# Kernel optimization log

Hardware: AMD Instinct MI355X
Metric: run time of the kernel (lower is better)

The kernel has to match this reference:

```python
import jax, jax.numpy as jnp
import numpy as np

HEADS = 8
DIM_HEAD = 64


def layernorm(x, g, b, eps=1e-5):
    mu = x.mean(axis=-1, keepdims=True)
    var = ((x - mu) ** 2).mean(axis=-1, keepdims=True)
    return (x - mu) * jax.lax.rsqrt(var + eps) * g + b


def setup_inputs() -> dict:
    key = jax.random.key(0)
    ks = jax.random.split(key, 8)
    B, N, D = 1, 896, 3072          # batch, enformer bins, enformer_hidden_dim
    C, J, CD = 64, 1, 2560          # num context tracks, kv len per track, context_dim
    INNER = HEADS * DIM_HEAD        # 512
    return {
        'embeddings': jax.random.normal(ks[0], (B, N, D), jnp.float32),
        'context': jax.random.normal(ks[1], (C, J, CD), jnp.float32),
        'context_mask': jnp.ones((C, J), dtype=bool),
        'qn_g': jnp.ones((D,), jnp.float32),
        'qn_b': jnp.zeros((D,), jnp.float32),
        'kn_g': jnp.ones((CD,), jnp.float32),
        'kn_b': jnp.zeros((CD,), jnp.float32),
        'Wq': jax.random.normal(ks[2], (D, INNER), jnp.float32) / np.sqrt(D),
        'Wkv': jax.random.normal(ks[3], (CD, 2 * INNER), jnp.float32) / np.sqrt(CD),
        'null_k': jax.random.normal(ks[4], (INNER,), jnp.float32),
        'null_v': jax.random.normal(ks[5], (INNER,), jnp.float32),
        'Wo': jax.random.normal(ks[6], (INNER, D), jnp.float32) / np.sqrt(INNER),
        'bo': jnp.zeros((D,), jnp.float32),
        'Wp': jax.random.normal(ks[7], (D, 1), jnp.float32) / np.sqrt(D),
        'bp': jnp.zeros((1,), jnp.float32),
    }


def reference(embeddings, context, context_mask, qn_g, qn_b, kn_g, kn_b,
              Wq, Wkv, null_k, null_v, Wo, bo, Wp, bp):
    h, dh = HEADS, DIM_HEAD
    scale = dh ** -0.5
    b, n, d = embeddings.shape
    c, j, _ = context.shape

    q = layernorm(embeddings, qn_g, qn_b) @ Wq                  # (b, n, h*dh)
    kv = layernorm(context, kn_g, kn_b) @ Wkv                   # (c, j, 2*h*dh)
    k, v = jnp.split(kv, 2, axis=-1)

    # null key/value concat along kv-sequence dim
    nk = jnp.broadcast_to(null_k, (c, 1, h * dh))
    nv = jnp.broadcast_to(null_v, (c, 1, h * dh))
    k = jnp.concatenate([nk, k], axis=1)                        # (c, j+1, h*dh)
    v = jnp.concatenate([nv, v], axis=1)

    q = q.reshape(b, n, h, dh).transpose(0, 2, 1, 3)            # (b, h, i, dh)
    k = k.reshape(c, j + 1, h, dh).transpose(0, 2, 1, 3)        # (c, h, j+1, dh)
    v = v.reshape(c, j + 1, h, dh).transpose(0, 2, 1, 3)

    sim = jnp.einsum('bhid,chjd->bchij', q, k) * scale          # (b, c, h, i, j+1)
    mask = jnp.pad(context_mask, ((0, 0), (1, 0)), constant_values=True)  # (c, j+1)
    sim = jnp.where(mask[None, :, None, None, :], sim, -jnp.finfo(sim.dtype).max)
    attn = jax.nn.softmax(sim, axis=-1)

    out = jnp.einsum('bchij,chjd->bchid', attn, v)              # (b, c, h, i, dh)
    out = out.transpose(0, 1, 3, 2, 4).reshape(b, c, n, h * dh)

    branch = out @ Wo + bo                                      # (b, c, n, d)
    emb2 = embeddings[:, None] + branch                         # residual (b==1 broadcast)

    pred = (emb2 @ Wp + bp)[..., 0]                             # (b, c, n)
    pred = jax.nn.softplus(pred).transpose(0, 2, 1)             # 'b c n 1 -> b n c'
    return pred
```

## Files before the change

### kernel.cpp

```cpp
#include <hip/hip_runtime.h>
#include <hip/hip_bf16.h>
#include <cstddef>

#define N_  896
#define D_  3072
#define C_  64
#define CD_ 2560
#define INNER_ 512
#define HEADS_ 8
#define ZQ_ 8
#define ZKV_ 8

typedef __attribute__((ext_vector_type(8))) short short8;
typedef __attribute__((ext_vector_type(4))) float f32x4;

__device__ __forceinline__ void split_bf16(float x, unsigned short& hi, unsigned short& lo)
{
    unsigned u = __float_as_uint(x);
    hi = (unsigned short)(u >> 16);
    float xh = __uint_as_float(u & 0xffff0000u);
    lo = (unsigned short)(__float_as_uint(x - xh) >> 16);
}

__global__ __launch_bounds__(256) void stats_wowp(
    const float* __restrict__ emb, const float* __restrict__ ctx,
    const float* __restrict__ Wp,  const float* __restrict__ Wo,
    const float* __restrict__ bo,  const float* __restrict__ bp,
    float2* __restrict__ statsE, float2* __restrict__ statsC,
    float* __restrict__ ep, float* __restrict__ WoWp, float* __restrict__ c0)
{
    const int bid = blockIdx.x;
    const int t = threadIdx.x;
    const int wave = t >> 6, lane = t & 63;
    __shared__ float sm[8];

    if (bid >= N_ + C_) {
        if (bid == N_ + C_ + 128) {
            float s = 0.f;
            for (int f = t; f < D_; f += 256) s += bo[f] * Wp[f];
#pragma unroll
            for (int off = 32; off > 0; off >>= 1) s += __shfl_xor(s, off);
            if (lane == 0) sm[wave] = s;
            __syncthreads();
            if (t == 0) c0[0] = sm[0] + sm[1] + sm[2] + sm[3] + bp[0];
        } else {
            const int row = (bid - (N_ + C_)) * 4 + wave;
            const float4* a4 = (const float4*)(Wo + (size_t)row * D_);
            const float4* w4 = (const float4*)Wp;
            float s = 0.f;
#pragma unroll
            for (int i = 0; i < 12; ++i) {
                const int f = lane + 64 * i;
                float4 a = a4[f], w = w4[f];
                s += a.x * w.x + a.y * w.y + a.z * w.z + a.w * w.w;
            }
#pragma unroll
            for (int off = 32; off > 0; off >>= 1) s += __shfl_xor(s, off);
            if (lane == 0) WoWp[row] = s;
        }
        return;
    }

    const bool isE = bid < N_;
    const int row = isE ? bid : bid - N_;
    const int ncols = isE ? D_ : CD_;
    const float* X = isE ? emb + (size_t)row * D_ : ctx + (size_t)row * CD_;
    const int nf4 = ncols >> 2;
    const float4* x4 = (const float4*)X;
    float4 xs[3];
    float sum = 0.f, dotp = 0.f;
#pragma unroll
    for (int i = 0; i < 3; ++i) {
        const int f = t + 256 * i;
        if (f < nf4) {
            float4 v = x4[f];
            xs[i] = v;
            sum += (v.x + v.y) + (v.z + v.w);
            if (isE) {
                float4 w = ((const float4*)Wp)[f];
                dotp += v.x * w.x + v.y * w.y + v.z * w.z + v.w * w.w;
            }
        }
    }
#pragma unroll
    for (int off = 32; off > 0; off >>= 1) {
        sum  += __shfl_xor(sum, off);
        dotp += __shfl_xor(dotp, off);
    }
    if (lane == 0) { sm[wave] = sum; sm[4 + wave] = dotp; }
    __syncthreads();
    sum  = sm[0] + sm[1] + sm[2] + sm[3];
    dotp = sm[4] + sm[5] + sm[6] + sm[7];
    const float mu = sum / (float)ncols;

    float sq = 0.f;
#pragma unroll
    for (int i = 0; i < 3; ++i) {
        const int f = t + 256 * i;
        if (f < nf4) {
            float4 v = xs[i];
            float a = v.x - mu, b2 = v.y - mu, c = v.z - mu, d = v.w - mu;
            sq += a * a + b2 * b2 + c * c + d * d;
        }
    }
#pragma unroll
    for (int off = 32; off > 0; off >>= 1) sq += __shfl_xor(sq, off);
    __syncthreads();
    if (lane == 0) sm[wave] = sq;
    __syncthreads();
    sq = sm[0] + sm[1] + sm[2] + sm[3];
    const float rstd = rsqrtf(sq / (float)ncols + 1e-5f);
    if (t == 0) {
        float2 st = make_float2(rstd, -mu * rstd);
        if (isE) { statsE[row] = st; ep[row] = dotp; }
        else     { statsC[row] = st; }
    }
}

__global__ __launch_bounds__(256) void gemms(
    const float* __restrict__ emb, const float2* __restrict__ statsE,
    const float* __restrict__ qg, const float* __restrict__ qb,
    const float* __restrict__ Wq, float* __restrict__ qpart,
    const float* __restrict__ ctx, const float2* __restrict__ statsC,
    const float* __restrict__ kg, const float* __restrict__ kb,
    const float* __restrict__ Wkv, float* __restrict__ kp)
{
    __shared__ __align__(16) char smem[44032];
    const int i = blockIdx.x;
    const int t = threadIdx.x;

    if (i < 224) {
        unsigned short (*Ah)[40] = (unsigned short (*)[40])(smem);
        unsigned short (*Al)[40] = (unsigned short (*)[40])(smem + 10240);
        unsigned short (*Bh)[40] = (unsigned short (*)[40])(smem + 20480);
        unsigned short (*Bl)[40] = (unsigned short (*)[40])(smem + 30720);
        float* gsl = (float*)(smem + 40960);
        float* bsl = gsl + 384;

        const int bz = i & 7, sp = i >> 3;
        const int bx = sp & 3, by = sp >> 2;
        const int m0 = by * 128, n0 = bx * 128, k0 = bz * 384;
        if (t < 96) {
            ((float4*)gsl)[t] = ((const float4*)(qg + k0))[t];
            ((float4*)bsl)[t] = ((const float4*)(qb + k0))[t];
        }
        const int ar = t >> 1;
        const int akk = (t & 1) << 4;
        const float2 st = statsE[m0 + ar];
        const int brp = t & 15;
        const int bn0 = (t >> 4) << 3;
        const int l = t & 63;
        const int w = t >> 6;
        const int wm = (w >> 1) << 6;
        const int wn = (w & 1) << 6;
        const int kk0 = (l >> 4) << 3;
        const int li = l & 15;

        const float* aP = emb + (size_t)(m0 + ar) * D_ + k0 + akk;
        const float* bP = Wq + (size_t)(k0 + 2 * brp) * INNER_ + n0 + bn0;
        float4 aR[4];
        float4 bRa0 = *(const float4*)bP;
        float4 bRa1 = *(const float4*)(bP + 4);
        float4 bRb0 = *(const float4*)(bP + INNER_);
        float4 bRb1 = *(const float4*)(bP + INNER_ + 4);
#pragma unroll
        for (int j = 0; j < 4; ++j) aR[j] = *(const float4*)(aP + 4 * j);

        f32x4 acc[4][4] = {};

        for (int itn = 0; itn < 12; ++itn) {
            __syncthreads();
            const int kbase = itn * 32 + akk;
#pragma unroll
            for (int j = 0; j < 4; ++j) {
                float xe[4] = {aR[j].x, aR[j].y, aR[j].z, aR[j].w};
                unsigned short h[4], lo[4];
#pragma unroll
                for (int e = 0; e < 4; ++e) {
                    const int kidx = kbase + 4 * j + e;
                    float x = (xe[e] * st.x + st.y) * gsl[kidx] + bsl[kidx];
                    split_bf16(x, h[e], lo[e]);
                }
                uint2 ph = make_uint2((unsigned)h[0] | ((unsigned)h[1] << 16),
                                      (unsigned)h[2] | ((unsigned)h[3] << 16));
                uint2 pl = make_uint2((unsigned)lo[0] | ((unsigned)lo[1] << 16),
                                      (unsigned)lo[2] | ((unsigned)lo[3] << 16));
                *(uint2*)&Ah[ar][akk + 4 * j] = ph;
                *(uint2*)&Al[ar][akk + 4 * j] = pl;
            }
            {
                float x0e[8] = {bRa0.x, bRa0.y, bRa0.z, bRa0.w, bRa1.x, bRa1.y, bRa1.z, bRa1.w};
                float x1e[8] = {bRb0.x, bRb0.y, bRb0.z, bRb0.w, bRb1.x, bRb1.y, bRb1.z, bRb1.w};
#pragma unroll
                for (int j = 0; j < 8; ++j) {
                    unsigned short h0, l0, h1, l1;
                    split_bf16(x0e[j], h0, l0);
                    split_bf16(x1e[j], h1, l1);
                    *(unsigned*)&Bh[bn0 + j][2 * brp] = (unsigned)h0 | ((unsigned)h1 << 16);
                    *(unsigned*)&Bl[bn0 + j][2 * brp] = (unsigned)l0 | ((unsigned)l1 << 16);
                }
            }
            if (itn < 11) {
                aP += 32;
                bP += (size_t)32 * INNER_;
                bRa0 = *(const float4*)bP;
                bRa1 = *(const float4*)(bP + 4);
                bRb0 = *(const float4*)(bP + INNER_);
                bRb1 = *(const float4*)(bP + INNER_ + 4);
#pragma unroll
                for (int j = 0; j < 4; ++j) aR[j] = *(const float4*)(aP + 4 * j);
            }
            __syncthreads();
            short8 bhf[4], blf[4];
#pragma unroll
            for (int fn = 0; fn < 4; ++fn) {
                const int rn = wn + fn * 16 + li;
                bhf[fn] = *(const short8*)&Bh[rn][kk0];
                blf[fn] = *(const short8*)&Bl[rn][kk0];
            }
#pragma unroll
            for (int fm = 0; fm < 4; ++fm) {
                const int rm = wm + fm * 16 + li;
                short8 ah = *(const short8*)&Ah[rm][kk0];
                short8 al = *(const short8*)&Al[rm][kk0];
#pragma unroll
                for (int fn = 0; fn < 4; ++fn) {
                    acc[fm][fn] = __builtin_amdgcn_mfma_f32_16x16x32_bf16(ah, bhf[fn], acc[fm][fn], 0, 0, 0);
                    acc[fm][fn] = __builtin_amdgcn_mfma_f32_16x16x32_bf16(ah, blf[fn], acc[fm][fn], 0, 0, 0);
                    acc[fm][fn] = __builtin_amdgcn_mfma_f32_16x16x32_bf16(al, bhf[fn], acc[fm][fn], 0, 0, 0);
                }
            }
        }
        float* Cp = qpart + (size_t)bz * (N_ * INNER_);
#pragma unroll
        for (int fm = 0; fm < 4; ++fm) {
            const int rbase = m0 + wm + fm * 16 + ((l >> 4) << 2);
#pragma unroll
            for (int fn = 0; fn < 4; ++fn) {
                const int col = n0 + wn + fn * 16 + li;
#pragma unroll
                for (int jj = 0; jj < 4; ++jj)
                    Cp[(size_t)(rbase + jj) * INNER_ + col] = acc[fm][fn][jj];
            }
        }
        return;
    }

    float (*As)[68] = (float (*)[68])(smem);
    float (*Bs)[68] = (float (*)[68])(smem + 8704);
    float* gs  = (float*)(smem + 17408);
    float* bs2 = gs + 320;
    const int j2 = i - 224;
    const int bz = j2 & 7;
    const int bx = j2 >> 3;
    const int n0 = bx * 64, k0 = bz * 320;
    float* Cc = kp + (size_t)bz * (C_ * 1024);

    for (int f = t; f < 80; f += 256) {
        ((float4*)gs)[f]  = ((const float4*)(kg + k0))[f];
        ((float4*)bs2)[f] = ((const float4*)(kb + k0))[f];
    }
    const int ar = t >> 2;
    const int ac = (t & 3) * 8;
    const float2 st = statsC[ar];
    const int bk = t >> 3;
    const int bn = (t & 7) * 8;
    const int tm = (t >> 4) * 4, tn = (t & 15) * 4;
    float acc[4][4] = {};

    for (int kt = k0; kt < k0 + 320; kt += 32) {
        const float* ap = ctx + (size_t)ar * CD_ + kt + ac;
        float4 a0 = *(const float4*)ap;
        float4 a1 = *(const float4*)(ap + 4);
        const float* bp2 = Wkv + (size_t)(kt + bk) * 1024 + n0 + bn;
        float4 b0 = *(const float4*)bp2;
        float4 b1 = *(const float4*)(bp2 + 4);
        __syncthreads();
        const int kr2 = kt - k0 + ac;
        float4 g0 = *(const float4*)&gs[kr2];
        float4 g1 = *(const float4*)&gs[kr2 + 4];
        float4 c0v = *(const float4*)&bs2[kr2];
        float4 c1v = *(const float4*)&bs2[kr2 + 4];
        As[ac + 0][ar] = (a0.x * st.x + st.y) * g0.x + c0v.x;
        As[ac + 1][ar] = (a0.y * st.x + st.y) * g0.y + c0v.y;
        As[ac + 2][ar] = (a0.z * st.x + st.y) * g0.z + c0v.z;
        As[ac + 3][ar] = (a0.w * st.x + st.y) * g0.w + c0v.w;
        As[ac + 4][ar] = (a1.x * st.x + st.y) * g1.x + c1v.x;
        As[ac + 5][ar] = (a1.y * st.x + st.y) * g1.y + c1v.y;
        As[ac + 6][ar] = (a1.z * st.x + st.y) * g1.z + c1v.z;
        As[ac + 7][ar] = (a1.w * st.x + st.y) * g1.w + c1v.w;
        *(float4*)&Bs[bk][bn]     = b0;
        *(float4*)&Bs[bk][bn + 4] = b1;
        __syncthreads();
#pragma unroll
        for (int kk = 0; kk < 32; ++kk) {
            float4 av = *(const float4*)&As[kk][tm];
            float4 bv = *(const float4*)&Bs[kk][tn];
            acc[0][0] += av.x * bv.x; acc[0][1] += av.x * bv.y;
            acc[0][2] += av.x * bv.z; acc[0][3] += av.x * bv.w;
            acc[1][0] += av.y * bv.x; acc[1][1] += av.y * bv.y;
            acc[1][2] += av.y * bv.z; acc[1][3] += av.y * bv.w;
            acc[2][0] += av.z * bv.x; acc[2][1] += av.z * bv.y;
            acc[2][2] += av.z * bv.z; acc[2][3] += av.z * bv.w;
            acc[3][0] += av.w * bv.x; acc[3][1] += av.w * bv.y;
            acc[3][2] += av.w * bv.z; acc[3][3] += av.w * bv.w;
        }
    }
#pragma unroll
    for (int r = 0; r < 4; ++r)
        *(float4*)(Cc + (size_t)(tm + r) * 1024 + n0 + tn) =
            make_float4(acc[r][0], acc[r][1], acc[r][2], acc[r][3]);
}

__global__ __launch_bounds__(256) void kred_vp(
    const float* __restrict__ kp, const float* __restrict__ WoWp,
    const float* __restrict__ null_v, float* __restrict__ kvb,
    float* __restrict__ vp, float* __restrict__ nvp)
{
    const int c = blockIdx.x;
    const int t = threadIdx.x;
#pragma unroll
    for (int n = t; n < 512; n += 256) {
        float s = 0.f;
#pragma unroll
        for (int z = 0; z < ZKV_; ++z) s += kp[(size_t)z * (C_ * 1024) + c * 1024 + n];
        kvb[c * 512 + n] = s;
    }
    const int w = t >> 6, lane = t & 63;
#pragma unroll
    for (int half = 0; half < 2; ++half) {
        const int jj = half * 256 + w * 64 + lane;
        float s = 0.f;
#pragma unroll
        for (int z = 0; z < ZKV_; ++z) s += kp[(size_t)z * (C_ * 1024) + c * 1024 + 512 + jj];
        float x = s * WoWp[jj];
#pragma unroll
        for (int off = 32; off > 0; off >>= 1) x += __shfl_xor(x, off);
        if (lane == 0) vp[c * 8 + half * 4 + w] = x;
    }
    if (c == 0) {
#pragma unroll
        for (int half = 0; half < 2; ++half) {
            const int jj = half * 256 + w * 64 + lane;
            float x = null_v[jj] * WoWp[jj];
#pragma unroll
            for (int off = 32; off > 0; off >>= 1) x += __shfl_xor(x, off);
            if (lane == 0) nvp[half * 4 + w] = x;
        }
    }
}

__global__ __launch_bounds__(512) void attn_pred(
    const float* __restrict__ qp, const float* __restrict__ kvb,
    const float* __restrict__ vp, const float* __restrict__ nvp,
    const float* __restrict__ nk, const float* __restrict__ ep,
    const float* __restrict__ c0p, const unsigned char* __restrict__ msk,
    float* __restrict__ out)
{
    const int t = threadIdx.x;
    const int n0 = blockIdx.x * 4;
    const size_t MN = (size_t)N_ * INNER_;
    __shared__ float q_lds[4][8][68];
    __shared__ float s0_lds[4][8];
#pragma unroll
    for (int nn = 0; nn < 4; ++nn) {
        const size_t base = (size_t)(n0 + nn) * INNER_ + t;
        float v = 0.f;
#pragma unroll
        for (int z = 0; z < ZQ_; ++z) v += qp[z * MN + base];
        q_lds[nn][t >> 6][t & 63] = v;
    }
    __syncthreads();
    if (t < 32) {
        const int nn = t >> 3, h = t & 7;
        const float* qq = &q_lds[nn][h][0];
        float s = 0.f;
#pragma unroll
        for (int d = 0; d < 64; ++d) s += qq[d] * nk[h * 64 + d];
        s0_lds[nn][h] = s * 0.125f;
    }
    __syncthreads();
    const int c = t >> 3, h = t & 7;
    const bool mv = (msk[c] != 0) || (msk[4 * c] != 0);
    float kreg[64];
    {
        const float4* k4 = (const float4*)(kvb + c * 512 + h * 64);
#pragma unroll
        for (int i = 0; i < 16; ++i) {
            float4 v = k4[i];
            kreg[4 * i] = v.x; kreg[4 * i + 1] = v.y;
            kreg[4 * i + 2] = v.z; kreg[4 * i + 3] = v.w;
        }
    }
    const float vpch = vp[c * 8 + h];
    const float nvph = nvp[h];
    const float c0 = c0p[0];
#pragma unroll
    for (int nn = 0; nn < 4; ++nn) {
        const float* qq = &q_lds[nn][h][0];
        float s = 0.f;
#pragma unroll
        for (int d = 0; d < 64; ++d) s += qq[d] * kreg[d];
        s *= 0.125f;
        float a1 = mv ? 1.f / (1.f + expf(s0_lds[nn][h] - s)) : 0.f;
        float contrib = nvph + a1 * (vpch - nvph);
        contrib += __shfl_xor(contrib, 1);
        contrib += __shfl_xor(contrib, 2);
        contrib += __shfl_xor(contrib, 4);
        if (h == 0) {
            float x = ep[n0 + nn] + c0 + contrib;
            out[(size_t)(n0 + nn) * 64 + c] = fmaxf(x, 0.f) + log1pf(expf(-fabsf(x)));
        }
    }
}

extern "C" void kernel_launch(void* const* d_in, const int* in_sizes, int n_in,
                              void* d_out, int out_size, void* d_ws, size_t ws_size,
                              hipStream_t stream)
{
    const float* emb    = (const float*)d_in[0];
    const float* ctx    = (const float*)d_in[1];
    const unsigned char* msk = (const unsigned char*)d_in[2];
    const float* qn_g   = (const float*)d_in[3];
    const float* qn_b   = (const float*)d_in[4];
    const float* kn_g   = (const float*)d_in[5];
    const float* kn_b   = (const float*)d_in[6];
    const float* Wq     = (const float*)d_in[7];
    const float* Wkv    = (const float*)d_in[8];
    const float* null_k = (const float*)d_in[9];
    const float* null_v = (const float*)d_in[10];
    const float* Wo     = (const float*)d_in[11];
    const float* bo     = (const float*)d_in[12];
    const float* Wp     = (const float*)d_in[13];
    const float* bp     = (const float*)d_in[14];
    float* out = (float*)d_out;

    float* ws    = (float*)d_ws;
    float* qpart = ws;
    float* kp    = qpart + (size_t)ZQ_ * N_ * INNER_;
    float* kvb   = kp + (size_t)ZKV_ * C_ * 1024;
    float* e_p   = kvb + (size_t)C_ * 512;
    float* WoWp  = e_p + N_;
    float* vp    = WoWp + INNER_;
    float* nvp   = vp + C_ * HEADS_;
    float* c0    = nvp + HEADS_;
    float2* statsE = (float2*)(c0 + 1);
    float2* statsC = statsE + N_;

    stats_wowp<<<N_ + C_ + 128 + 1, 256, 0, stream>>>(
        emb, ctx, Wp, Wo, bo, bp, statsE, statsC, e_p, WoWp, c0);
    gemms<<<224 + 16 * ZKV_, 256, 0, stream>>>(
        emb, statsE, qn_g, qn_b, Wq, qpart,
        ctx, statsC, kn_g, kn_b, Wkv, kp);
    kred_vp<<<C_, 256, 0, stream>>>(kp, WoWp, null_v, kvb, vp, nvp);
    attn_pred<<<N_ / 4, 512, 0, stream>>>(qpart, kvb, vp, nvp, null_k,
                                          e_p, c0, msk, out);
}
```

Baseline: 140.7 us.

## Move context KV projection onto split-bf16 MFMA path with shared GEMM helper

The context LayerNorm+Wkv projection, previously a scalar FP32 SIMT GEMM with 128 blocks at 8-way split-K, now reuses the same 3-pass split-bf16 MFMA routine as the query projection. It runs as 32 blocks of 128x128 tiles with 4-way split-K and rows clamped and masked for the 64 real rows. The bf16 hi/lo split also switches from truncation to round-to-nearest-even. The KV tiles waste half their MFMA work on padding rows, and the grid shrinks to 256 blocks.

Measured after the change: 157.4 us. 11.9% more time.

```diff
diff --git a/kernel.cpp b/kernel.cpp
--- a/kernel.cpp
+++ b/kernel.cpp
@@ -9,17 +9,19 @@
 #define INNER_ 512
 #define HEADS_ 8
 #define ZQ_ 8
-#define ZKV_ 8
+#define ZKV_ 4
 
 typedef __attribute__((ext_vector_type(8))) short short8;
 typedef __attribute__((ext_vector_type(4))) float f32x4;
 
-__device__ __forceinline__ void split_bf16(float x, unsigned short& hi, unsigned short& lo)
+__device__ __forceinline__ void split_bf16_rne(float x, unsigned short& hi, unsigned short& lo)
 {
     unsigned u = __float_as_uint(x);
-    hi = (unsigned short)(u >> 16);
-    float xh = __uint_as_float(u & 0xffff0000u);
-    lo = (unsigned short)(__float_as_uint(x - xh) >> 16);
+    unsigned short h = (unsigned short)((u + 0x7fffu + ((u >> 16) & 1u)) >> 16);
+    float xh = __uint_as_float((unsigned)h << 16);
+    unsigned ur = __float_as_uint(x - xh);
+    unsigned short l2 = (unsigned short)((ur + 0x7fffu + ((ur >> 16) & 1u)) >> 16);
+    hi = h; lo = l2;
 }
 
 __global__ __launch_bounds__(256) void stats_wowp(
@@ -117,6 +119,128 @@
     }
 }
 
+__device__ __forceinline__ void mfma_gemm_ln(
+    char* smem, int t,
+    const float* __restrict__ A, int lda, const float2* __restrict__ stats, int Mreal,
+    const float* __restrict__ gv, const float* __restrict__ bv,
+    const float* __restrict__ Bm, int ldb,
+    float* __restrict__ Cp, int ldc,
+    int m0, int n0, int k0, int iters)
+{
+    unsigned short (*Ah)[40] = (unsigned short (*)[40])(smem);
+    unsigned short (*Al)[40] = (unsigned short (*)[40])(smem + 10240);
+    unsigned short (*Bh)[40] = (unsigned short (*)[40])(smem + 20480);
+    unsigned short (*Bl)[40] = (unsigned short (*)[40])(smem + 30720);
+    float* gsl = (float*)(smem + 40960);
+    float* bsl = gsl + 640;
+
+    for (int f = t; f < iters * 8; f += 256) {
+        ((float4*)gsl)[f] = ((const float4*)(gv + k0))[f];
+        ((float4*)bsl)[f] = ((const float4*)(bv + k0))[f];
+    }
+    const int ar  = t >> 1;
+    const int akk = (t & 1) << 4;
+    const int arow = min(m0 + ar, Mreal - 1);
+    const float2 st = stats[arow];
+    const int brp = t & 15;
+    const int bn0 = (t >> 4) << 3;
+    const int l  = t & 63;
+    const int w  = t >> 6;
+    const int wm = (w >> 1) << 6;
+    const int wn = (w & 1) << 6;
+    const int kk0 = (l >> 4) << 3;
+    const int li  = l & 15;
+
+    const float* aP = A + (size_t)arow * lda + k0 + akk;
+    const float* bP = Bm + (size_t)(k0 + 2 * brp) * ldb + n0 + bn0;
+    float4 aR[4], bR[4];
+    bR[0] = *(const float4*)bP;
+    bR[1] = *(const float4*)(bP + 4);
+    bR[2] = *(const float4*)(bP + ldb);
+    bR[3] = *(const float4*)(bP + ldb + 4);
+#pragma unroll
+    for (int j = 0; j < 4; ++j) aR[j] = *(const float4*)(aP + 4 * j);
+
+    f32x4 acc[4][4] = {};
+
+    for (int itn = 0; itn < iters; ++itn) {
+        __syncthreads();
+        const int kbase = itn * 32 + akk;
+#pragma unroll
+        for (int j = 0; j < 4; ++j) {
+            float xe[4] = {aR[j].x, aR[j].y, aR[j].z, aR[j].w};
+            unsigned short h[4], lo[4];
+#pragma unroll
+            for (int e = 0; e < 4; ++e) {
+                const int kidx = kbase + 4 * j + e;
+                float x = (xe[e] * st.x + st.y) * gsl[kidx] + bsl[kidx];
+                split_bf16_rne(x, h[e], lo[e]);
+            }
+            uint2 ph = make_uint2((unsigned)h[0] | ((unsigned)h[1] << 16),
+                                  (unsigned)h[2] | ((unsigned)h[3] << 16));
+            uint2 pl = make_uint2((unsigned)lo[0] | ((unsigned)lo[1] << 16),
+                                  (unsigned)lo[2] | ((unsigned)lo[3] << 16));
+            *(uint2*)&Ah[ar][akk + 4 * j] = ph;
+            *(uint2*)&Al[ar][akk + 4 * j] = pl;
+        }
+        {
+            float x0e[8] = {bR[0].x, bR[0].y, bR[0].z, bR[0].w, bR[1].x, bR[1].y, bR[1].z, bR[1].w};
+            float x1e[8] = {bR[2].x, bR[2].y, bR[2].z, bR[2].w, bR[3].x, bR[3].y, bR[3].z, bR[3].w};
+#pragma unroll
+            for (int j = 0; j < 8; ++j) {
+                unsigned short h0, l0, h1, l1;
+                split_bf16_rne(x0e[j], h0, l0);
+                split_bf16_rne(x1e[j], h1, l1);
+                *(unsigned*)&Bh[bn0 + j][2 * brp] = (unsigned)h0 | ((unsigned)h1 << 16);
+                *(unsigned*)&Bl[bn0 + j][2 * brp] = (unsigned)l0 | ((unsigned)l1 << 16);
+            }
+        }
+        if (itn < iters - 1) {
+            aP += 32;
+            bP += (size_t)32 * ldb;
+            bR[0] = *(const float4*)bP;
+            bR[1] = *(const float4*)(bP + 4);
+            bR[2] = *(const float4*)(bP + ldb);
+            bR[3] = *(const float4*)(bP + ldb + 4);
+#pragma unroll
+            for (int j = 0; j < 4; ++j) aR[j] = *(const float4*)(aP + 4 * j);
+        }
+        __syncthreads();
+        short8 bhf[4], blf[4];
+#pragma unroll
+        for (int fn = 0; fn < 4; ++fn) {
+            const int rn = wn + fn * 16 + li;
+            bhf[fn] = *(const short8*)&Bh[rn][kk0];
+            blf[fn] = *(const short8*)&Bl[rn][kk0];
+        }
+#pragma unroll
+        for (int fm = 0; fm < 4; ++fm) {
+            const int rm = wm + fm * 16 + li;
+            short8 ah = *(const short8*)&Ah[rm][kk0];
+            short8 al = *(const short8*)&Al[rm][kk0];
+#pragma unroll
+            for (int fn = 0; fn < 4; ++fn) {
+                acc[fm][fn] = __builtin_amdgcn_mfma_f32_16x16x32_bf16(ah, bhf[fn], acc[fm][fn], 0, 0, 0);
+                acc[fm][fn] = __builtin_amdgcn_mfma_f32_16x16x32_bf16(ah, blf[fn], acc[fm][fn], 0, 0, 0);
+                acc[fm][fn] = __builtin_amdgcn_mfma_f32_16x16x32_bf16(al, bhf[fn], acc[fm][fn], 0, 0, 0);
+            }
+        }
+    }
+#pragma unroll
+    for (int fm = 0; fm < 4; ++fm) {
+        const int trow = wm + fm * 16 + ((l >> 4) << 2);
+        if (m0 + trow < Mreal) {
+#pragma unroll
+            for (int fn = 0; fn < 4; ++fn) {
+                const int col = n0 + wn + fn * 16 + li;
+#pragma unroll
+                for (int jj = 0; jj < 4; ++jj)
+                    Cp[(size_t)(m0 + trow + jj) * ldc + col] = acc[fm][fn][jj];
+            }
+        }
+    }
+}
+
 __global__ __launch_bounds__(256) void gemms(
     const float* __restrict__ emb, const float2* __restrict__ statsE,
     const float* __restrict__ qg, const float* __restrict__ qb,
@@ -125,191 +249,22 @@
     const float* __restrict__ kg, const float* __restrict__ kb,
     const float* __restrict__ Wkv, float* __restrict__ kp)
 {
-    __shared__ __align__(16) char smem[44032];
+    __shared__ __align__(16) char smem[46080];
     const int i = blockIdx.x;
     const int t = threadIdx.x;
-
     if (i < 224) {
-        unsigned short (*Ah)[40] = (unsigned short (*)[40])(smem);
-        unsigned short (*Al)[40] = (unsigned short (*)[40])(smem + 10240);
-        unsigned short (*Bh)[40] = (unsigned short (*)[40])(smem + 20480);
-        unsigned short (*Bl)[40] = (unsigned short (*)[40])(smem + 30720);
-        float* gsl = (float*)(smem + 40960);
-        float* bsl = gsl + 384;
-
         const int bz = i & 7, sp = i >> 3;
         const int bx = sp & 3, by = sp >> 2;
-        const int m0 = by * 128, n0 = bx * 128, k0 = bz * 384;
-        if (t < 96) {
-            ((float4*)gsl)[t] = ((const float4*)(qg + k0))[t];
-            ((float4*)bsl)[t] = ((const float4*)(qb + k0))[t];
-        }
-        const int ar = t >> 1;
-        const int akk = (t & 1) << 4;
-        const float2 st = statsE[m0 + ar];
-        const int brp = t & 15;
-        const int bn0 = (t >> 4) << 3;
-        const int l = t & 63;
-        const int w = t >> 6;
-        const int wm = (w >> 1) << 6;
-        const int wn = (w & 1) << 6;
-        const int kk0 = (l >> 4) << 3;
-        const int li = l & 15;
-
-        const float* aP = emb + (size_t)(m0 + ar) * D_ + k0 + akk;
-        const float* bP = Wq + (size_t)(k0 + 2 * brp) * INNER_ + n0 + bn0;
-        float4 aR[4];
-        float4 bRa0 = *(const float4*)bP;
-        float4 bRa1 = *(const float4*)(bP + 4);
-        float4 bRb0 = *(const float4*)(bP + INNER_);
-        float4 bRb1 = *(const float4*)(bP + INNER_ + 4);
-#pragma unroll
-        for (int j = 0; j < 4; ++j) aR[j] = *(const float4*)(aP + 4 * j);
-
-        f32x4 acc[4][4] = {};
-
-        for (int itn = 0; itn < 12; ++itn) {
-            __syncthreads();
-            const int kbase = itn * 32 + akk;
-#pragma unroll
-            for (int j = 0; j < 4; ++j) {
-                float xe[4] = {aR[j].x, aR[j].y, aR[j].z, aR[j].w};
-                unsigned short h[4], lo[4];
-#pragma unroll
-                for (int e = 0; e < 4; ++e) {
-                    const int kidx = kbase + 4 * j + e;
-                    float x = (xe[e] * st.x + st.y) * gsl[kidx] + bsl[kidx];
-                    split_bf16(x, h[e], lo[e]);
-                }
-                uint2 ph = make_uint2((unsigned)h[0] | ((unsigned)h[1] << 16),
-                                      (unsigned)h[2] | ((unsigned)h[3] << 16));
-                uint2 pl = make_uint2((unsigned)lo[0] | ((unsigned)lo[1] << 16),
-                                      (unsigned)lo[2] | ((unsigned)lo[3] << 16));
-                *(uint2*)&Ah[ar][akk + 4 * j] = ph;
-                *(uint2*)&Al[ar][akk + 4 * j] = pl;
-            }
-            {
-                float x0e[8] = {bRa0.x, bRa0.y, bRa0.z, bRa0.w, bRa1.x, bRa1.y, bRa1.z, bRa1.w};
-                float x1e[8] = {bRb0.x, bRb0.y, bRb0.z, bRb0.w, bRb1.x, bRb1.y, bRb1.z, bRb1.w};
-#pragma unroll
-                for (int j = 0; j < 8; ++j) {
-                    unsigned short h0, l0, h1, l1;
-                    split_bf16(x0e[j], h0, l0);
-                    split_bf16(x1e[j], h1, l1);
-                    *(unsigned*)&Bh[bn0 + j][2 * brp] = (unsigned)h0 | ((unsigned)h1 << 16);
-                    *(unsigned*)&Bl[bn0 + j][2 * brp] = (unsigned)l0 | ((unsigned)l1 << 16);
-                }
-            }
-            if (itn < 11) {
-                aP += 32;
-                bP += (size_t)32 * INNER_;
-                bRa0 = *(const float4*)bP;
-                bRa1 = *(const float4*)(bP + 4);
-                bRb0 = *(const float4*)(bP + INNER_);
-                bRb1 = *(const float4*)(bP + INNER_ + 4);
-#pragma unroll
-                for (int j = 0; j < 4; ++j) aR[j] = *(const float4*)(aP + 4 * j);
-            }
-            __syncthreads();
-            short8 bhf[4], blf[4];
-#pragma unroll
-            for (int fn = 0; fn < 4; ++fn) {
-                const int rn = wn + fn * 16 + li;
-                bhf[fn] = *(const short8*)&Bh[rn][kk0];
-                blf[fn] = *(const short8*)&Bl[rn][kk0];
-            }
-#pragma unroll
-            for (int fm = 0; fm < 4; ++fm) {
-                const int rm = wm + fm * 16 + li;
-                short8 ah = *(const short8*)&Ah[rm][kk0];
-                short8 al = *(const short8*)&Al[rm][kk0];
-#pragma unroll
-                for (int fn = 0; fn < 4; ++fn) {
-                    acc[fm][fn] = __builtin_amdgcn_mfma_f32_16x16x32_bf16(ah, bhf[fn], acc[fm][fn], 0, 0, 0);
-                    acc[fm][fn] = __builtin_amdgcn_mfma_f32_16x16x32_bf16(ah, blf[fn], acc[fm][fn], 0, 0, 0);
-                    acc[fm][fn] = __builtin_amdgcn_mfma_f32_16x16x32_bf16(al, bhf[fn], acc[fm][fn], 0, 0, 0);
-                }
-            }
-        }
-        float* Cp = qpart + (size_t)bz * (N_ * INNER_);
-#pragma unroll
-        for (int fm = 0; fm < 4; ++fm) {
-            const int rbase = m0 + wm + fm * 16 + ((l >> 4) << 2);
-#pragma unroll
-            for (int fn = 0; fn < 4; ++fn) {
-                const int col = n0 + wn + fn * 16 + li;
-#pragma unroll
-                for (int jj = 0; jj < 4; ++jj)
-                    Cp[(size_t)(rbase + jj) * INNER_ + col] = acc[fm][fn][jj];
-            }
-        }
-        return;
-    }
-
-    float (*As)[68] = (float (*)[68])(smem);
-    float (*Bs)[68] = (float (*)[68])(smem + 8704);
-    float* gs  = (float*)(smem + 17408);
-    float* bs2 = gs + 320;
-    const int j2 = i - 224;
-    const int bz = j2 & 7;
-    const int bx = j2 >> 3;
-    const int n0 = bx * 64, k0 = bz * 320;
-    float* Cc = kp + (size_t)bz * (C_ * 1024);
-
-    for (int f = t; f < 80; f += 256) {
-        ((float4*)gs)[f]  = ((const float4*)(kg + k0))[f];
-        ((float4*)bs2)[f] = ((const float4*)(kb + k0))[f];
-    }
-    const int ar = t >> 2;
-    const int ac = (t & 3) * 8;
-    const float2 st = statsC[ar];
-    const int bk = t >> 3;
-    const int bn = (t & 7) * 8;
-    const int tm = (t >> 4) * 4, tn = (t & 15) * 4;
-    float acc[4][4] = {};
-
-    for (int kt = k0; kt < k0 + 320; kt += 32) {
-        const float* ap = ctx + (size_t)ar * CD_ + kt + ac;
-        float4 a0 = *(const float4*)ap;
-        float4 a1 = *(const float4*)(ap + 4);
-        const float* bp2 = Wkv + (size_t)(kt + bk) * 1024 + n0 + bn;
-        float4 b0 = *(const float4*)bp2;
-        float4 b1 = *(const float4*)(bp2 + 4);
-        __syncthreads();
-        const int kr2 = kt - k0 + ac;
-        float4 g0 = *(const float4*)&gs[kr2];
-        float4 g1 = *(const float4*)&gs[kr2 + 4];
-        float4 c0v = *(const float4*)&bs2[kr2];
-        float4 c1v = *(const float4*)&bs2[kr2 + 4];
-        As[ac + 0][ar] = (a0.x * st.x + st.y) * g0.x + c0v.x;
-        As[ac + 1][ar] = (a0.y * st.x + st.y) * g0.y + c0v.y;
-        As[ac + 2][ar] = (a0.z * st.x + st.y) * g0.z + c0v.z;
-        As[ac + 3][ar] = (a0.w * st.x + st.y) * g0.w + c0v.w;
-        As[ac + 4][ar] = (a1.x * st.x + st.y) * g1.x + c1v.x;
-        As[ac + 5][ar] = (a1.y * st.x + st.y) * g1.y + c1v.y;
-        As[ac + 6][ar] = (a1.z * st.x + st.y) * g1.z + c1v.z;
-        As[ac + 7][ar] = (a1.w * st.x + st.y) * g1.w + c1v.w;
-        *(float4*)&Bs[bk][bn]     = b0;
-        *(float4*)&Bs[bk][bn + 4] = b1;
-        __syncthreads();
-#pragma unroll
-        for (int kk = 0; kk < 32; ++kk) {
-            float4 av = *(const float4*)&As[kk][tm];
-            float4 bv = *(const float4*)&Bs[kk][tn];
-            acc[0][0] += av.x * bv.x; acc[0][1] += av.x * bv.y;
-            acc[0][2] += av.x * bv.z; acc[0][3] += av.x * bv.w;
-            acc[1][0] += av.y * bv.x; acc[1][1] += av.y * bv.y;
-            acc[1][2] += av.y * bv.z; acc[1][3] += av.y * bv.w;
-            acc[2][0] += av.z * bv.x; acc[2][1] += av.z * bv.y;
-            acc[2][2] += av.z * bv.z; acc[2][3] += av.z * bv.w;
-            acc[3][0] += av.w * bv.x; acc[3][1] += av.w * bv.y;
-            acc[3][2] += av.w * bv.z; acc[3][3] += av.w * bv.w;
-        }
-    }
-#pragma unroll
-    for (int r = 0; r < 4; ++r)
-        *(float4*)(Cc + (size_t)(tm + r) * 1024 + n0 + tn) =
-            make_float4(acc[r][0], acc[r][1], acc[r][2], acc[r][3]);
+        mfma_gemm_ln(smem, t, emb, D_, statsE, N_, qg, qb, Wq, INNER_,
+                     qpart + (size_t)bz * (N_ * INNER_), INNER_,
+                     by * 128, bx * 128, bz * 384, 12);
+    } else {
+        const int j2 = i - 224;
+        const int bz = j2 & 3, bx = j2 >> 2;
+        mfma_gemm_ln(smem, t, ctx, CD_, statsC, C_, kg, kb, Wkv, 1024,
+                     kp + (size_t)bz * (C_ * 1024), 1024,
+                     0, bx * 128, bz * 640, 20);
+    }
 }
 
 __global__ __launch_bounds__(256) void kred_vp(
@@ -449,7 +404,7 @@
 
     stats_wowp<<<N_ + C_ + 128 + 1, 256, 0, stream>>>(
         emb, ctx, Wp, Wo, bo, bp, statsE, statsC, e_p, WoWp, c0);
-    gemms<<<224 + 16 * ZKV_, 256, 0, stream>>>(
+    gemms<<<256, 256, 0, stream>>>(
         emb, statsE, qn_g, qn_b, Wq, qpart,
         ctx, statsC, kn_g, kn_b, Wkv, kp);
     kred_vp<<<C_, 256, 0, stream>>>(kp, WoWp, null_v, kvb, vp, nvp);
```
